# Kernel tuning notes

Measured on AMD Instinct MI355X. Metric: run time of the kernel, lower is better.

The kernel has to match this reference:

```python
import jax, jax.numpy as jnp
import numpy as np

N, P, M, J, H = 32768, 5, 1024, 24, 256
SMPL_THRESH = 0.08


def _rand_transforms(rng, n):
    # random small-angle rotations + small translations -> invertible 4x4 joint transforms
    axis = rng.normal(size=(n, 3))
    axis /= np.linalg.norm(axis, axis=-1, keepdims=True)
    ang = rng.uniform(-0.5, 0.5, size=(n, 1, 1))
    K = np.zeros((n, 3, 3))
    K[:, 0, 1] = -axis[:, 2]; K[:, 0, 2] = axis[:, 1]
    K[:, 1, 0] = axis[:, 2];  K[:, 1, 2] = -axis[:, 0]
    K[:, 2, 0] = -axis[:, 1]; K[:, 2, 1] = axis[:, 0]
    R = np.eye(3)[None] + np.sin(ang) * K + (1.0 - np.cos(ang)) * (K @ K)
    T = np.zeros((n, 4, 4))
    T[:, :3, :3] = R
    T[:, :3, 3] = rng.normal(size=(n, 3)) * 0.1
    T[:, 3, 3] = 1.0
    return T.astype(np.float32)


def setup_inputs() -> dict:
    key = jax.random.key(0)
    ks = jax.random.split(key, 12)
    rng = np.random.default_rng(0)
    pose_pts = jax.random.normal(ks[0], (1, N, 3), jnp.float32) * 0.5
    pose_dirs = jax.random.normal(ks[1], (1, N, 3), jnp.float32)
    pose_dirs = pose_dirs / jnp.linalg.norm(pose_dirs, axis=-1, keepdims=True)
    part_pts = jax.random.normal(ks[2], (P, M, 3), jnp.float32) * 0.5
    part_pbw = jax.nn.softmax(jax.random.normal(ks[3], (P, M, J), jnp.float32), axis=-1)
    A = jnp.asarray(_rand_transforms(rng, J))[None]       # [1,24,4,4]
    big_A = jnp.asarray(_rand_transforms(rng, J))[None]   # [1,24,4,4]
    W1 = jax.random.normal(ks[4], (3, H), jnp.float32) * 0.1
    b1 = jnp.zeros((H,), jnp.float32)
    W2 = jax.random.normal(ks[5], (H, H), jnp.float32) * 0.06
    b2 = jnp.zeros((H,), jnp.float32)
    W3 = jax.random.normal(ks[6], (H, 3), jnp.float32) * 0.06
    b3 = jnp.zeros((3,), jnp.float32)
    lengths2 = jnp.full((P,), M, dtype=jnp.int32)
    return {"pose_pts": pose_pts, "pose_dirs": pose_dirs, "part_pts": part_pts,
            "part_pbw": part_pbw, "A": A, "big_A": big_A,
            "W1": W1, "b1": b1, "W2": W2, "b2": b2, "W3": W3, "b3": b3,
            "lengths2": lengths2}


def _lbs_pipeline(pose_pts, pose_dirs, part_pts, part_pbw, A, big_A,
                  W1, b1, W2, b2, W3, b3, lengths2):
    # ---- KNN (K=1) blend-weight lookup per part (torch.no_grad block) ----
    x = pose_pts[0]                                              # [N,3]
    d2 = (jnp.sum(x * x, -1)[:, None, None]
          - 2.0 * jnp.einsum('nd,pmd->npm', x, part_pts)
          + jnp.sum(part_pts * part_pts, -1)[None])              # [N,P,M]
    valid = jnp.arange(M)[None, :] < lengths2[:, None]           # [P,M]
    d2 = jnp.where(valid[None], jnp.maximum(d2, 0.0), jnp.inf)
    nn = jnp.argmin(d2, axis=-1)                                 # [N,P]
    pnorm = jnp.sqrt(jnp.take_along_axis(d2, nn[..., None], -1)[..., 0])  # [N,P]
    bw = part_pbw[jnp.arange(P)[None, :], nn]                    # [N,P,24]
    bw = jax.lax.stop_gradient(bw)
    pnorm = jax.lax.stop_gradient(pnorm)
    pflag = pnorm < SMPL_THRESH                                  # [N,P]

    # ---- gather-expand: each point assigned to every part ----
    pts_e = jnp.broadcast_to(x[:, None, :], (N, P, 3)).reshape(N * P, 3)
    dirs_e = jnp.broadcast_to(pose_dirs[0][:, None, :], (N, P, 3)).reshape(N * P, 3)
    bw_f = bw.reshape(N * P, J)

    # ---- per-point inverse linear blend skinning ----
    A_bw = jnp.einsum('kj,jxy->kxy', bw_f, A[0])                 # [NP,4,4]
    R_inv = jnp.linalg.inv(A_bw[:, :3, :3])
    tpts = jnp.einsum('kxy,ky->kx', R_inv, pts_e - A_bw[:, :3, 3])
    Ab = jnp.einsum('kj,jxy->kxy', bw_f, big_A[0])               # [NP,4,4]
    Rb = Ab[:, :3, :3]
    init_bigpose = jnp.einsum('kxy,ky->kx', Rb, tpts) + Ab[:, :3, 3]
    tdirs = jnp.einsum('kxy,ky->kx', R_inv, dirs_e)
    tpose_dirs = jnp.einsum('kxy,ky->kx', Rb, tdirs).reshape(1, N, P, 3)

    # ---- tpose deformer (residual MLP, masked by part flag) ----
    h = jax.nn.relu(init_bigpose @ W1 + b1)
    h = jax.nn.relu(h @ W2 + b2)
    resd = 0.05 * jnp.tanh(h @ W3 + b3)
    resd = resd * pflag.reshape(N * P, 1).astype(resd.dtype)
    tpose = (init_bigpose + resd).reshape(1, N, P, 3)
    return (tpose, tpose_dirs, resd.reshape(1, N, P, 3),
            pflag.reshape(1, N, P), init_bigpose[None], pnorm[None])


def reference(pose_pts, pose_dirs, part_pts, part_pbw, A, big_A,
              W1, b1, W2, b2, W3, b3, lengths2):
    return _lbs_pipeline(pose_pts, pose_dirs, part_pts, part_pbw, A, big_A,
                         W1, b1, W2, b2, W3, b3, lengths2)
```

## Files before the change

### kernel.cpp

```cpp
#include <hip/hip_runtime.h>
#include <stdint.h>
#include <math.h>

#define NPTS 32768
#define PP   5
#define MM   1024
#define JJ   24
#define HH   256

#define O0 0
#define O1 491520
#define O2 983040
#define O3 1474560
#define O4 1638400
#define O5 2129920

typedef unsigned short ushort_t;
typedef unsigned int   uint_t;
typedef unsigned long long u64_t;
typedef __attribute__((ext_vector_type(8))) short bf16x8;
typedef __attribute__((ext_vector_type(4))) float f32x4;

__device__ __forceinline__ ushort_t f2bf(float f) {
  union { uint_t i; float f; } v; v.f = f;
  uint_t i = v.i;
  return (ushort_t)((i + 0x7FFFu + ((i >> 16) & 1u)) >> 16);
}
__device__ __forceinline__ uint_t cvt_pk_bf16(float lo, float hi) {
  uint_t r;
  asm("v_cvt_pk_bf16_f32 %0, %1, %2" : "=v"(r) : "v"(lo), "v"(hi));
  return r;
}
__device__ __forceinline__ float tanh_fast(float v) {
  v = fminf(fmaxf(v, -15.f), 15.f);
  float e = __expf(2.f*v);
  return __fdividef(e - 1.f, e + 1.f);
}

__global__ __launch_bounds__(256) void prep_w2(const float* __restrict__ W2g,
                                               ushort_t* __restrict__ W2bf)
{
  int k = blockIdx.x;
  int n = threadIdx.x;
  float v = W2g[k*256 + n];
  int kc = k >> 5, quad = (k & 31) >> 3, j = k & 7;
  int tile = n >> 4, lane = quad*16 + (n & 15);
  W2bf[kc*8192 + tile*512 + lane*8 + j] = f2bf(v);
}

__device__ __forceinline__ void transform_one(
    int n, int p, int nn, float pn, float fl,
    float px, float py, float pz, float dx, float dy, float dz,
    const float* __restrict__ pbw,
    const float4* __restrict__ sA4, const float4* __restrict__ sB4,
    float* __restrict__ out)
{
  const float4* bwr = (const float4*)(pbw + ((size_t)p * MM + nn) * JJ);
  float bw[24];
  #pragma unroll
  for (int q = 0; q < 6; ++q) {
    float4 u = bwr[q];
    bw[q*4+0] = u.x; bw[q*4+1] = u.y; bw[q*4+2] = u.z; bw[q*4+3] = u.w;
  }

  float M1[12], M2[12];
  #pragma unroll
  for (int q = 0; q < 12; ++q) { M1[q] = 0.f; M2[q] = 0.f; }
  #pragma unroll
  for (int j = 0; j < 24; ++j) {
    float w = bw[j];
    float4 a0 = sA4[j*3+0], a1 = sA4[j*3+1], a2 = sA4[j*3+2];
    M1[0]=fmaf(w,a0.x,M1[0]); M1[1]=fmaf(w,a0.y,M1[1]); M1[2]=fmaf(w,a0.z,M1[2]); M1[3]=fmaf(w,a0.w,M1[3]);
    M1[4]=fmaf(w,a1.x,M1[4]); M1[5]=fmaf(w,a1.y,M1[5]); M1[6]=fmaf(w,a1.z,M1[6]); M1[7]=fmaf(w,a1.w,M1[7]);
    M1[8]=fmaf(w,a2.x,M1[8]); M1[9]=fmaf(w,a2.y,M1[9]); M1[10]=fmaf(w,a2.z,M1[10]); M1[11]=fmaf(w,a2.w,M1[11]);
    float4 c0 = sB4[j*3+0], c1 = sB4[j*3+1], c2 = sB4[j*3+2];
    M2[0]=fmaf(w,c0.x,M2[0]); M2[1]=fmaf(w,c0.y,M2[1]); M2[2]=fmaf(w,c0.z,M2[2]); M2[3]=fmaf(w,c0.w,M2[3]);
    M2[4]=fmaf(w,c1.x,M2[4]); M2[5]=fmaf(w,c1.y,M2[5]); M2[6]=fmaf(w,c1.z,M2[6]); M2[7]=fmaf(w,c1.w,M2[7]);
    M2[8]=fmaf(w,c2.x,M2[8]); M2[9]=fmaf(w,c2.y,M2[9]); M2[10]=fmaf(w,c2.z,M2[10]); M2[11]=fmaf(w,c2.w,M2[11]);
  }
  float a=M1[0], b=M1[1], c=M1[2];
  float d=M1[4], e=M1[5], f=M1[6];
  float g=M1[8], h=M1[9], i=M1[10];
  float C00 = e*i - f*h, C01 = c*h - b*i, C02 = b*f - c*e;
  float C10 = f*g - d*i, C11 = a*i - c*g, C12 = c*d - a*f;
  float C20 = d*h - e*g, C21 = b*g - a*h, C22 = a*e - b*d;
  float det = a*C00 + b*C10 + c*C20;
  float rd = 1.0f / det;
  float tx = px - M1[3], ty = py - M1[7], tz = pz - M1[11];
  float t0 = rd * (C00*tx + C01*ty + C02*tz);
  float t1 = rd * (C10*tx + C11*ty + C12*tz);
  float t2 = rd * (C20*tx + C21*ty + C22*tz);
  float i0 = M2[0]*t0 + M2[1]*t1 + M2[2]*t2  + M2[3];
  float i1 = M2[4]*t0 + M2[5]*t1 + M2[6]*t2  + M2[7];
  float i2 = M2[8]*t0 + M2[9]*t1 + M2[10]*t2 + M2[11];
  float d0 = rd * (C00*dx + C01*dy + C02*dz);
  float d1 = rd * (C10*dx + C11*dy + C12*dz);
  float d2 = rd * (C20*dx + C21*dy + C22*dz);
  float e0 = M2[0]*d0 + M2[1]*d1 + M2[2]*d2;
  float e1 = M2[4]*d0 + M2[5]*d1 + M2[6]*d2;
  float e2 = M2[8]*d0 + M2[9]*d1 + M2[10]*d2;

  size_t k = (size_t)n * PP + p;
  out[O1 + k*3+0] = e0; out[O1 + k*3+1] = e1; out[O1 + k*3+2] = e2;
  out[O3 + k] = fl;
  out[O4 + k*3+0] = i0; out[O4 + k*3+1] = i1; out[O4 + k*3+2] = i2;
  out[O5 + k] = pn;
}

__global__ __launch_bounds__(256) void nn_kernel(
    const float* __restrict__ pp0, const float* __restrict__ pp1,
    const float* __restrict__ part_pts, const float* __restrict__ pbw,
    const float* __restrict__ Ag, const float* __restrict__ Bg,
    const int* __restrict__ lengths2, float* __restrict__ out)
{
  __shared__ float4 sPart[MM];
  __shared__ float4 sA4[72];
  __shared__ float4 sB4[72];
  int t = threadIdx.x;
  int p  = blockIdx.x >> 8;
  int nb = blockIdx.x & 255;
  int g  = t >> 3;
  int s  = t & 7;
  int n0 = nb*128 + g*4;

  float s0r0 = pp0[0], s0r1 = pp0[1], s0r2 = pp0[2];
  float nrm = s0r0*s0r0 + s0r1*s0r1 + s0r2*s0r2;
  bool c0_is_dirs = fabsf(nrm - 1.0f) < 1e-4f;
  const float* pose_pts  = c0_is_dirs ? pp1 : pp0;
  const float* pose_dirs = c0_is_dirs ? pp0 : pp1;

  {
    #pragma clang fp contract(off)
    for (int i = t; i < MM; i += 256) {
      float x = part_pts[((size_t)p*MM+i)*3+0];
      float y = part_pts[((size_t)p*MM+i)*3+1];
      float z = part_pts[((size_t)p*MM+i)*3+2];
      float yy = ((x*x) + (y*y)) + (z*z);
      sPart[i] = make_float4(x, y, z, yy);
    }
  }
  for (int i = t; i < 72; i += 256) {
    int l = i*4;
    int j = l / 12, rc = l % 12;
    float4 qa, qb;
    qa.x = Ag[j*16+rc+0]; qa.y = Ag[j*16+rc+1]; qa.z = Ag[j*16+rc+2]; qa.w = Ag[j*16+rc+3];
    qb.x = Bg[j*16+rc+0]; qb.y = Bg[j*16+rc+1]; qb.z = Bg[j*16+rc+2]; qb.w = Bg[j*16+rc+3];
    sA4[i] = qa; sB4[i] = qb;
  }
  int mlen = lengths2[p]; if (mlen > MM) mlen = MM;
  __syncthreads();

  float X[4], Y[4], Z[4], X2[4];
  {
    #pragma clang fp contract(off)
    const float4* pr = (const float4*)(pose_pts + (size_t)n0*3);
    float4 f0 = pr[0], f1 = pr[1], f2 = pr[2];
    X[0]=f0.x; Y[0]=f0.y; Z[0]=f0.z;
    X[1]=f0.w; Y[1]=f1.x; Z[1]=f1.y;
    X[2]=f1.z; Y[2]=f1.w; Z[2]=f2.x;
    X[3]=f2.y; Y[3]=f2.z; Z[3]=f2.w;
    #pragma unroll
    for (int j = 0; j < 4; ++j)
      X2[j] = ((X[j]*X[j]) + (Y[j]*Y[j])) + (Z[j]*Z[j]);
  }

  float best[4] = {INFINITY, INFINITY, INFINITY, INFINITY};
  int   code[4] = {0, 0, 0, 0};
  {
    #pragma clang fp contract(off)
    int mb = 0;
    for (; mb + 63 < mlen; mb += 64) {
      float4 q[8];
      #pragma unroll
      for (int i = 0; i < 8; ++i) q[i] = sPart[mb + s + 8*i];
      #pragma unroll
      for (int i = 0; i < 8; ++i) {
        int c = (mb >> 3) + i;
        #pragma unroll
        for (int j = 0; j < 4; ++j) {
          float dt = ((X[j]*q[i].x) + (Y[j]*q[i].y)) + (Z[j]*q[i].z);
          float dd = fmaxf((X2[j] - (2.0f*dt)) + q[i].w, 0.0f);
          bool lt = dd < best[j];
          best[j] = fminf(best[j], dd);
          code[j] = lt ? c : code[j];
        }
      }
    }
    for (int m = mb + s; m < mlen; m += 8) {
      float4 q = sPart[m];
      int c = (m - s) >> 3;
      #pragma unroll
      for (int j = 0; j < 4; ++j) {
        float dt = ((X[j]*q.x) + (Y[j]*q.y)) + (Z[j]*q.z);
        float dd = fmaxf((X2[j] - (2.0f*dt)) + q.w, 0.0f);
        bool lt = dd < best[j];
        best[j] = fminf(best[j], dd);
        code[j] = lt ? c : code[j];
      }
    }
  }

  u64_t pk[4];
  #pragma unroll
  for (int j = 0; j < 4; ++j) {
    pk[j] = ((u64_t)__float_as_uint(best[j]) << 32) | (uint_t)(code[j]*8 + s);
    u64_t o;
    o = __shfl_xor(pk[j], 1); if (o < pk[j]) pk[j] = o;
    o = __shfl_xor(pk[j], 2); if (o < pk[j]) pk[j] = o;
    o = __shfl_xor(pk[j], 4); if (o < pk[j]) pk[j] = o;
  }

  if (s < 4) {
    u64_t mypk = (s==0) ? pk[0] : (s==1) ? pk[1] : (s==2) ? pk[2] : pk[3];
    float xa = (s==0) ? X[0] : (s==1) ? X[1] : (s==2) ? X[2] : X[3];
    float ya = (s==0) ? Y[0] : (s==1) ? Y[1] : (s==2) ? Y[2] : Y[3];
    float za = (s==0) ? Z[0] : (s==1) ? Z[1] : (s==2) ? Z[2] : Z[3];
    int n = n0 + s;
    int bm = (int)(mypk & 0xFFFFFFFFull);
    float bd = __uint_as_float((uint_t)(mypk >> 32));
    float pn = sqrtf(bd);
    float fl = ((double)pn < 0.08) ? 1.0f : 0.0f;
    float dxa = pose_dirs[n*3+0], dya = pose_dirs[n*3+1], dza = pose_dirs[n*3+2];
    transform_one(n, p, bm, pn, fl, xa, ya, za, dxa, dya, dza, pbw, sA4, sB4, out);
  }
}

__global__ __launch_bounds__(256) void mlp_kernel(
    const float* __restrict__ W1g, const float* __restrict__ b1g,
    const float* __restrict__ b2g, const float* __restrict__ W3g,
    const float* __restrict__ b3g, const ushort_t* __restrict__ W2bf,
    float* __restrict__ out)
{
  __shared__ struct {
    ushort_t B[2][8192];
    float4   w1c[256];
    float4   w3b2[256];
  } sm;

  int t = threadIdx.x;
  int wave = t >> 6, lane = t & 63, quad = lane >> 4, m16 = lane & 15;
  size_t row0 = (size_t)blockIdx.x * 64 + (size_t)wave * 16;

  auto stage = [&](int buf, int kc) {
    const ushort_t* src = W2bf + kc*8192 + wave*2048 + lane*8;
    #pragma unroll
    for (int i = 0; i < 4; ++i) {
      __builtin_amdgcn_global_load_lds(
        (const __attribute__((address_space(1))) void*)(src + i*512),
        (__attribute__((address_space(3))) void*)(&sm.B[buf][wave*2048 + i*512]),
        16, 0, 0);
    }
  };
  stage(0, 0);

  {
    int c = t;
    sm.w1c[c]  = make_float4(W1g[c], W1g[256+c], W1g[512+c], b1g[c]);
    sm.w3b2[c] = make_float4(W3g[c*3+0], W3g[c*3+1], W3g[c*3+2], b2g[c]);
  }

  int r0 = (int)row0 + m16;
  float x0 = out[O4 + (size_t)r0*3+0], y0 = out[O4 + (size_t)r0*3+1], z0 = out[O4 + (size_t)r0*3+2];

  f32x4 acc0[16];
  #pragma unroll
  for (int nt = 0; nt < 16; ++nt) acc0[nt] = (f32x4){0.f,0.f,0.f,0.f};

  int cur = 0;
  for (int kc = 0; kc < 8; ++kc) {
    asm volatile("s_waitcnt vmcnt(0)" ::: "memory");
    __syncthreads();
    if (kc < 7) stage(cur ^ 1, kc + 1);

    union { bf16x8 v; uint_t u[4]; } ua0;
    int c0 = kc*32 + quad*8;
    #pragma unroll
    for (int jj = 0; jj < 4; ++jj) {
      float4 wA = sm.w1c[c0 + 2*jj];
      float4 wB = sm.w1c[c0 + 2*jj + 1];
      float hA0 = fmaxf(fmaf(z0, wA.z, fmaf(y0, wA.y, fmaf(x0, wA.x, wA.w))), 0.f);
      float hB0 = fmaxf(fmaf(z0, wB.z, fmaf(y0, wB.y, fmaf(x0, wB.x, wB.w))), 0.f);
      ua0.u[jj] = cvt_pk_bf16(hA0, hB0);
    }

    const ushort_t* Bk = &sm.B[cur][lane*8];
    #pragma unroll
    for (int nt = 0; nt < 16; ++nt) {
      bf16x8 Bw = *(const bf16x8*)(Bk + nt*512);
      acc0[nt] = __builtin_amdgcn_mfma_f32_16x16x32_bf16(ua0.v, Bw, acc0[nt], 0, 0, 0);
    }
    cur ^= 1;
  }

  float flv = out[O3 + row0 + (size_t)m16];
  float ivx = out[O4 + (row0 + (size_t)m16)*3 + 0];
  float ivy = out[O4 + (row0 + (size_t)m16)*3 + 1];
  float ivz = out[O4 + (row0 + (size_t)m16)*3 + 2];

  float pr[4][3];
  #pragma unroll
  for (int reg = 0; reg < 4; ++reg) { pr[reg][0]=0.f; pr[reg][1]=0.f; pr[reg][2]=0.f; }
  #pragma unroll
  for (int nt = 0; nt < 16; ++nt) {
    float4 cv = sm.w3b2[nt*16 + m16];
    #pragma unroll
    for (int reg = 0; reg < 4; ++reg) {
      float h2 = fmaxf(acc0[nt][reg] + cv.w, 0.f);
      pr[reg][0] = fmaf(h2, cv.x, pr[reg][0]);
      pr[reg][1] = fmaf(h2, cv.y, pr[reg][1]);
      pr[reg][2] = fmaf(h2, cv.z, pr[reg][2]);
    }
  }
  float b30 = b3g[0], b31 = b3g[1], b32 = b3g[2];
  #pragma unroll
  for (int reg = 0; reg < 4; ++reg) {
    float p0 = pr[reg][0], p1 = pr[reg][1], p2 = pr[reg][2];
    #pragma unroll
    for (int mask = 1; mask < 16; mask <<= 1) {
      p0 += __shfl_xor(p0, mask);
      p1 += __shfl_xor(p1, mask);
      p2 += __shfl_xor(p2, mask);
    }
    int src = quad*4 + reg;
    float fl = __shfl(flv, src);
    float i0 = __shfl(ivx, src);
    float i1 = __shfl(ivy, src);
    float i2 = __shfl(ivz, src);
    if (m16 == 0) {
      int r = (int)row0 + src;
      float rr0 = 0.05f * tanh_fast(p0 + b30) * fl;
      float rr1 = 0.05f * tanh_fast(p1 + b31) * fl;
      float rr2 = 0.05f * tanh_fast(p2 + b32) * fl;
      out[O0 + (size_t)r*3+0] = i0 + rr0;
      out[O0 + (size_t)r*3+1] = i1 + rr1;
      out[O0 + (size_t)r*3+2] = i2 + rr2;
      out[O2 + (size_t)r*3+0] = rr0;
      out[O2 + (size_t)r*3+1] = rr1;
      out[O2 + (size_t)r*3+2] = rr2;
    }
  }
}

extern "C" void kernel_launch(void* const* d_in, const int* in_sizes, int n_in,
                              void* d_out, int out_size, void* d_ws, size_t ws_size,
                              hipStream_t stream) {
  (void)out_size; (void)ws_size;
  const int want[13] = {98304, 98304, 15360, 122880, 384, 384, 768, 256, 65536, 256, 768, 3, 5};
  int idx[13];
  bool used[64] = {false};
  for (int L = 0; L < 13; ++L) {
    idx[L] = -1;
    for (int s = 0; s < n_in && s < 64; ++s) {
      if (!used[s] && in_sizes[s] == want[L]) { idx[L] = s; used[s] = true; break; }
    }
    if (idx[L] < 0) idx[L] = L;
  }
  const float* pp0       = (const float*)d_in[idx[0]];
  const float* pp1       = (const float*)d_in[idx[1]];
  const float* part_pts  = (const float*)d_in[idx[2]];
  const float* part_pbw  = (const float*)d_in[idx[3]];
  const float* A         = (const float*)d_in[idx[4]];
  const float* bigA      = (const float*)d_in[idx[5]];
  const float* W1        = (const float*)d_in[idx[6]];
  const float* b1        = (const float*)d_in[idx[7]];
  const float* W2        = (const float*)d_in[idx[8]];
  const float* b2        = (const float*)d_in[idx[9]];
  const float* W3        = (const float*)d_in[idx[10]];
  const float* b3        = (const float*)d_in[idx[11]];
  const int*   lengths2  = (const int*)d_in[idx[12]];
  float* out = (float*)d_out;
  ushort_t* W2bf = (ushort_t*)d_ws;

  prep_w2<<<256, 256, 0, stream>>>(W2, W2bf);
  nn_kernel<<<1280, 256, 0, stream>>>(pp0, pp1, part_pts, part_pbw,
                                      A, bigA, lengths2, out);
  mlp_kernel<<<2560, 256, 0, stream>>>(W1, b1, b2, W3, b3, W2bf, out);
}
```

Measured before the change: 188.9 us.

## Fold W2 prep into NN kernel and vectorize NN search with SoA packed math

The separate W2 bf16 repack kernel is merged into the nearest-neighbour kernel as 256 extra blocks, which removes one launch. Part points are now stored in LDS as structure-of-arrays, so each thread reads four consecutive points per float4 and evaluates them with two-wide float vectors, letting the compiler emit packed FP32 math. The distance expression is algebraically reordered (2x folded into the query coordinates), and the point-to-index mapping changes to keep argmin tie order consistent. Rounding may differ slightly from the reference because of the reordering.

```diff
diff --git a/kernel.cpp b/kernel.cpp
--- a/kernel.cpp
+++ b/kernel.cpp
@@ -20,6 +20,7 @@
 typedef unsigned long long u64_t;
 typedef __attribute__((ext_vector_type(8))) short bf16x8;
 typedef __attribute__((ext_vector_type(4))) float f32x4;
+typedef __attribute__((ext_vector_type(2))) float f32x2;
 
 __device__ __forceinline__ ushort_t f2bf(float f) {
   union { uint_t i; float f; } v; v.f = f;
@@ -35,17 +36,6 @@
   v = fminf(fmaxf(v, -15.f), 15.f);
   float e = __expf(2.f*v);
   return __fdividef(e - 1.f, e + 1.f);
-}
-
-__global__ __launch_bounds__(256) void prep_w2(const float* __restrict__ W2g,
-                                               ushort_t* __restrict__ W2bf)
-{
-  int k = blockIdx.x;
-  int n = threadIdx.x;
-  float v = W2g[k*256 + n];
-  int kc = k >> 5, quad = (k & 31) >> 3, j = k & 7;
-  int tile = n >> 4, lane = quad*16 + (n & 15);
-  W2bf[kc*8192 + tile*512 + lane*8 + j] = f2bf(v);
 }
 
 __device__ __forceinline__ void transform_one(
@@ -111,9 +101,21 @@
     const float* __restrict__ pp0, const float* __restrict__ pp1,
     const float* __restrict__ part_pts, const float* __restrict__ pbw,
     const float* __restrict__ Ag, const float* __restrict__ Bg,
-    const int* __restrict__ lengths2, float* __restrict__ out)
+    const int* __restrict__ lengths2,
+    const float* __restrict__ W2g, ushort_t* __restrict__ W2bf,
+    float* __restrict__ out)
 {
-  __shared__ float4 sPart[MM];
+  if (blockIdx.x >= 1280) {
+    int k = blockIdx.x - 1280;
+    int n = threadIdx.x;
+    float v = W2g[k*256 + n];
+    int kc = k >> 5, quad = (k & 31) >> 3, j = k & 7;
+    int tile = n >> 4, lane = quad*16 + (n & 15);
+    W2bf[kc*8192 + tile*512 + lane*8 + j] = f2bf(v);
+    return;
+  }
+
+  __shared__ float4 sXq[256], sYq[256], sZq[256], sWq[256];
   __shared__ float4 sA4[72];
   __shared__ float4 sB4[72];
   int t = threadIdx.x;
@@ -131,12 +133,14 @@
 
   {
     #pragma clang fp contract(off)
+    float* fX = (float*)sXq; float* fY = (float*)sYq;
+    float* fZ = (float*)sZq; float* fW = (float*)sWq;
     for (int i = t; i < MM; i += 256) {
       float x = part_pts[((size_t)p*MM+i)*3+0];
       float y = part_pts[((size_t)p*MM+i)*3+1];
       float z = part_pts[((size_t)p*MM+i)*3+2];
       float yy = ((x*x) + (y*y)) + (z*z);
-      sPart[i] = make_float4(x, y, z, yy);
+      fX[i] = x; fY[i] = y; fZ[i] = z; fW[i] = yy;
     }
   }
   for (int i = t; i < 72; i += 256) {
@@ -150,7 +154,8 @@
   int mlen = lengths2[p]; if (mlen > MM) mlen = MM;
   __syncthreads();
 
-  float X[4], Y[4], Z[4], X2[4];
+  float X[4], Y[4], Z[4];
+  f32x2 Xd[4], Yd[4], Zd[4], C2[4];
   {
     #pragma clang fp contract(off)
     const float4* pr = (const float4*)(pose_pts + (size_t)n0*3);
@@ -160,50 +165,72 @@
     X[2]=f1.z; Y[2]=f1.w; Z[2]=f2.x;
     X[3]=f2.y; Y[3]=f2.z; Z[3]=f2.w;
     #pragma unroll
-    for (int j = 0; j < 4; ++j)
-      X2[j] = ((X[j]*X[j]) + (Y[j]*Y[j])) + (Z[j]*Z[j]);
+    for (int j = 0; j < 4; ++j) {
+      float x2 = ((X[j]*X[j]) + (Y[j]*Y[j])) + (Z[j]*Z[j]);
+      Xd[j] = (f32x2){2.0f*X[j], 2.0f*X[j]};
+      Yd[j] = (f32x2){2.0f*Y[j], 2.0f*Y[j]};
+      Zd[j] = (f32x2){2.0f*Z[j], 2.0f*Z[j]};
+      C2[j] = (f32x2){x2, x2};
+    }
   }
 
   float best[4] = {INFINITY, INFINITY, INFINITY, INFINITY};
   int   code[4] = {0, 0, 0, 0};
   {
     #pragma clang fp contract(off)
-    int mb = 0;
-    for (; mb + 63 < mlen; mb += 64) {
-      float4 q[8];
+    int nq = mlen >> 5;
+    for (int k = 0; k < nq; ++k) {
+      int qi = k*8 + s;
+      float4 QX = sXq[qi], QY = sYq[qi], QZ = sZq[qi], QW = sWq[qi];
+      f32x2 qx0 = {QX.x, QX.y}, qx1 = {QX.z, QX.w};
+      f32x2 qy0 = {QY.x, QY.y}, qy1 = {QY.z, QY.w};
+      f32x2 qz0 = {QZ.x, QZ.y}, qz1 = {QZ.z, QZ.w};
+      f32x2 qw0 = {QW.x, QW.y}, qw1 = {QW.z, QW.w};
+      int cb = k << 2;
       #pragma unroll
-      for (int i = 0; i < 8; ++i) q[i] = sPart[mb + s + 8*i];
+      for (int j = 0; j < 4; ++j) {
+        f32x2 dt0 = ((Xd[j]*qx0) + (Yd[j]*qy0)) + (Zd[j]*qz0);
+        f32x2 tt0 = (C2[j] - dt0) + qw0;
+        f32x2 dt1 = ((Xd[j]*qx1) + (Yd[j]*qy1)) + (Zd[j]*qz1);
+        f32x2 tt1 = (C2[j] - dt1) + qw1;
+        float e0 = fmaxf(tt0.x, 0.f);
+        float e1 = fmaxf(tt0.y, 0.f);
+        float e2 = fmaxf(tt1.x, 0.f);
+        float e3 = fmaxf(tt1.y, 0.f);
+        bool l0 = e0 < best[j]; best[j] = fminf(best[j], e0); code[j] = l0 ? cb       : code[j];
+        bool l1 = e1 < best[j]; best[j] = fminf(best[j], e1); code[j] = l1 ? (cb | 1) : code[j];
+        bool l2 = e2 < best[j]; best[j] = fminf(best[j], e2); code[j] = l2 ? (cb | 2) : code[j];
+        bool l3 = e3 < best[j]; best[j] = fminf(best[j], e3); code[j] = l3 ? (cb | 3) : code[j];
+      }
+    }
+    int mb0 = nq << 5;
+    if (mb0 < mlen) {
+      const float* fX = (const float*)sXq; const float* fY = (const float*)sYq;
+      const float* fZ = (const float*)sZq; const float* fW = (const float*)sWq;
       #pragma unroll
-      for (int i = 0; i < 8; ++i) {
-        int c = (mb >> 3) + i;
-        #pragma unroll
-        for (int j = 0; j < 4; ++j) {
-          float dt = ((X[j]*q[i].x) + (Y[j]*q[i].y)) + (Z[j]*q[i].z);
-          float dd = fmaxf((X2[j] - (2.0f*dt)) + q[i].w, 0.0f);
-          bool lt = dd < best[j];
-          best[j] = fminf(best[j], dd);
-          code[j] = lt ? c : code[j];
+      for (int e = 0; e < 4; ++e) {
+        int m = mb0 + 4*s + e;
+        if (m < mlen) {
+          float qx = fX[m], qy = fY[m], qz = fZ[m], qw = fW[m];
+          int cc = (nq << 2) | e;
+          #pragma unroll
+          for (int j = 0; j < 4; ++j) {
+            float dt2 = ((Xd[j].x*qx) + (Yd[j].x*qy)) + (Zd[j].x*qz);
+            float dd = fmaxf((C2[j].x - dt2) + qw, 0.0f);
+            bool lt = dd < best[j];
+            best[j] = fminf(best[j], dd);
+            code[j] = lt ? cc : code[j];
+          }
         }
       }
     }
-    for (int m = mb + s; m < mlen; m += 8) {
-      float4 q = sPart[m];
-      int c = (m - s) >> 3;
-      #pragma unroll
-      for (int j = 0; j < 4; ++j) {
-        float dt = ((X[j]*q.x) + (Y[j]*q.y)) + (Z[j]*q.z);
-        float dd = fmaxf((X2[j] - (2.0f*dt)) + q.w, 0.0f);
-        bool lt = dd < best[j];
-        best[j] = fminf(best[j], dd);
-        code[j] = lt ? c : code[j];
-      }
-    }
   }
 
   u64_t pk[4];
   #pragma unroll
   for (int j = 0; j < 4; ++j) {
-    pk[j] = ((u64_t)__float_as_uint(best[j]) << 32) | (uint_t)(code[j]*8 + s);
+    int mj = ((code[j] >> 2) << 5) + 4*s + (code[j] & 3);
+    pk[j] = ((u64_t)__float_as_uint(best[j]) << 32) | (uint_t)mj;
     u64_t o;
     o = __shfl_xor(pk[j], 1); if (o < pk[j]) pk[j] = o;
     o = __shfl_xor(pk[j], 2); if (o < pk[j]) pk[j] = o;
@@ -371,8 +398,7 @@
   float* out = (float*)d_out;
   ushort_t* W2bf = (ushort_t*)d_ws;
 
-  prep_w2<<<256, 256, 0, stream>>>(W2, W2bf);
-  nn_kernel<<<1280, 256, 0, stream>>>(pp0, pp1, part_pts, part_pbw,
-                                      A, bigA, lengths2, out);
+  nn_kernel<<<1536, 256, 0, stream>>>(pp0, pp1, part_pts, part_pbw,
+                                      A, bigA, lengths2, W2, W2bf, out);
   mlp_kernel<<<2560, 256, 0, stream>>>(W1, b1, b2, W3, b3, W2bf, out);
 }
```

Result: faster. 176.8 us (-6.4%).
